# Kernel tuning notes

Measured on AMD Instinct MI355X. Metric: run time of the kernel, lower is better.

The kernel has to match this reference:

```python
import jax, jax.numpy as jnp
import numpy as np
from jax import lax

A = -0.75  # torch bicubic cubic-kernel coefficient

def _cubic(t):
    t = jnp.abs(t)
    return jnp.where(t <= 1.0, ((A + 2.0) * t - (A + 3.0)) * t * t + 1.0,
                     jnp.where(t < 2.0, A * (((t - 5.0) * t + 8.0) * t - 4.0), 0.0))

def _up2_1d(x, axis):
    # torch F.interpolate(scale_factor=2, mode='bicubic', align_corners=False) along one axis
    n = x.shape[axis]
    src = (jnp.arange(2 * n, dtype=jnp.float32) + 0.5) / 2.0 - 0.5
    i0 = jnp.floor(src).astype(jnp.int32)
    taps = i0[:, None] + jnp.arange(-1, 3)          # [2n,4]
    w = _cubic(src[:, None] - taps.astype(jnp.float32))
    g = jnp.take(x, jnp.clip(taps, 0, n - 1), axis=axis)  # clamp = border replicate
    wshape = [1] * g.ndim
    wshape[axis] = 2 * n
    wshape[axis + 1] = 4
    return jnp.sum(g * w.reshape(wshape), axis=axis + 1)

def bicubic_x2(x):
    return _up2_1d(_up2_1d(x, 2), 3)

def conv2d(x, w, b, stride=1, pad=0):
    y = lax.conv_general_dilated(x, w, (stride, stride), [(pad, pad), (pad, pad)],
                                 dimension_numbers=('NCHW', 'OIHW', 'NCHW'))
    return y + b[None, :, None, None]

def lrelu(x):
    return jax.nn.leaky_relu(x, 0.2)

def resblock(x, w1, b1, w2, b2):
    return x + conv2d(jax.nn.relu(conv2d(x, w1, b1, pad=1)), w2, b2, pad=1)

def feat_head(x, cw, cb, rw1, rb1, rw2, rb2):
    # Conv2d(3,32,5,p=2) -> LReLU -> ResBlock(32) -> LReLU
    return lrelu(resblock(lrelu(conv2d(x, cw, cb, pad=2)), rw1, rb1, rw2, rb2))

def setup_inputs() -> dict:
    key = jax.random.key(0)
    ks = jax.random.split(key, 16)
    def w(k, shape):
        fan = shape[1] * shape[2] * shape[3]
        return jax.random.normal(k, shape, jnp.float32) / np.sqrt(fan)
    def bvec(k, n):
        return jax.random.normal(k, (n,), jnp.float32) * 0.01
    return {
        'x':     jax.random.normal(ks[0], (1, 64, 320, 320), jnp.float32),
        'query': jax.random.normal(ks[1], (1, 3, 160, 160), jnp.float32),
        'ref':   jax.random.normal(ks[2], (1, 3, 320, 320), jnp.float32),
        'conv1_w': w(ks[3], (32, 3, 5, 5)),   'conv1_b': bvec(ks[4], 32),
        'r1_w1':   w(ks[5], (32, 32, 3, 3)),  'r1_b1':   bvec(ks[6], 32),
        'r1_w2':   w(ks[7], (32, 32, 3, 3)),  'r1_b2':   bvec(ks[8], 32),
        'p1_w':    w(ks[9], (32, 64, 5, 5)),  'p1_b':    bvec(ks[10], 32),
        'pr_w1':   w(ks[11], (32, 32, 3, 3)), 'pr_b1':   bvec(ks[12], 32),
        'pr_w2':   w(ks[13], (32, 32, 3, 3)), 'pr_b2':   bvec(ks[14], 32),
        'p2_w':    w(ks[15], (3, 32, 1, 1)),  'p2_b':    jnp.zeros((3,), jnp.float32),
    }

def reference(x, query, ref, conv1_w, conv1_b, r1_w1, r1_b1, r1_w2, r1_b2,
              p1_w, p1_b, pr_w1, pr_b1, pr_w2, pr_b2, p2_w, p2_b):
    ks = 2
    qf = feat_head(bicubic_x2(query), conv1_w, conv1_b, r1_w1, r1_b1, r1_w2, r1_b2)
    rf = feat_head(ref, conv1_w, conv1_b, r1_w1, r1_b1, r1_w2, r1_b2)
    feat = jnp.concatenate([rf, qf], axis=1)  # [b,64,h,w]
    hid = lrelu(resblock(lrelu(conv2d(feat, p1_w, p1_b, pad=2)), pr_w1, pr_b1, pr_w2, pr_b2))
    affine = conv2d(hid, p2_w, p2_b, pad=0) + 1.0   # [b,3,h,w]
    affine = jnp.clip(affine, -3.0, 3.0)
    xp = jnp.pad(x, ((0, 0), (0, 0), (1, 1), (1, 1)), mode='reflect')
    b, c, hp, wp = xp.shape
    h, w = affine.shape[2], affine.shape[3]
    aff = jnp.transpose(affine, (0, 2, 3, 1))       # [b,h,w,3]
    s_x, s_y = aff[..., 0:1], aff[..., 1:2]
    theta = (aff[..., 2:3] - 1.0) * 1.0472          # +/- 60 degrees
    # kernel grid (ks=2): meshgrid('ij') of [-0.5, 0.5], flattened
    pn_x = jnp.array([-0.5, -0.5, 0.5, 0.5], dtype=xp.dtype)
    pn_y = jnp.array([-0.5, 0.5, -0.5, 0.5], dtype=xp.dtype)
    px = pn_x * s_x                                  # [b,h,w,4]
    py = pn_y * s_y
    ct, st = jnp.cos(theta), jnp.sin(theta)
    # [px,py] @ [[c, s],[-s, c]]
    rx = px * ct - py * st
    ry = px * st + py * ct
    off = (ks - 1) // 2 + 0.5                        # 0.5
    p0x = jnp.arange(1, h + 1, dtype=xp.dtype)[None, :, None, None]
    p0y = jnp.arange(1, w + 1, dtype=xp.dtype)[None, None, :, None]
    p_x = rx + off + p0x
    p_y = ry + off + p0y
    lt_x = jnp.floor(lax.stop_gradient(p_x))
    lt_y = jnp.floor(lax.stop_gradient(p_y))
    rb_x, rb_y = lt_x + 1.0, lt_y + 1.0
    lt_xc = jnp.clip(lt_x, 0, hp - 1); lt_yc = jnp.clip(lt_y, 0, wp - 1)
    rb_xc = jnp.clip(rb_x, 0, hp - 1); rb_yc = jnp.clip(rb_y, 0, wp - 1)
    p_x = jnp.clip(p_x, 0, hp - 1); p_y = jnp.clip(p_y, 0, wp - 1)
    g_lt = (1.0 + lt_xc - p_x) * (1.0 + lt_yc - p_y)
    g_rb = (1.0 - (rb_xc - p_x)) * (1.0 - (rb_yc - p_y))
    g_lb = (1.0 + lt_xc - p_x) * (1.0 - (rb_yc - p_y))
    g_rt = (1.0 - (rb_xc - p_x)) * (1.0 + lt_yc - p_y)
    x_flat = xp.reshape(b, c, hp * wp)
    def gather(qx, qy):
        idx = qx.astype(jnp.int32) * wp + qy.astype(jnp.int32)  # [b,h,w,4]
        return jax.vmap(lambda xf, ix: xf[:, ix])(x_flat, idx)   # [b,c,h,w,4]
    align = (g_lt[:, None] * gather(lt_xc, lt_yc)
             + g_rb[:, None] * gather(rb_xc, rb_yc)
             + g_lb[:, None] * gather(lt_xc, rb_yc)
             + g_rt[:, None] * gather(rb_xc, lt_yc))
    # pixel-shuffle style reshape: N index = ix*ks + iy (from 'ij' meshgrid)
    out = align.reshape(b, c, h, w, ks, ks).transpose(0, 1, 2, 4, 3, 5).reshape(b, c, h * ks, w * ks)
    return out
```

## Files before the change

### kernel.cpp

```cpp
#include <hip/hip_runtime.h>

#define H 320
#define W 320
#define HW (H * W)
#define CH 64

typedef _Float16 f16;
typedef _Float16 f16x8 __attribute__((ext_vector_type(8)));
typedef float f32x16 __attribute__((ext_vector_type(16)));

__device__ __forceinline__ float cubw(float t) {
    t = fabsf(t);
    if (t <= 1.f) return (1.25f * t - 2.25f) * t * t + 1.f;
    if (t < 2.f)  return -0.75f * (((t - 5.f) * t + 8.f) * t - 4.f);
    return 0.f;
}

__global__ __launch_bounds__(256) void bicubic_k(const float* __restrict__ q,
                                                 float* __restrict__ outp) {
    int idx = blockIdx.x * 256 + threadIdx.x;
    if (idx >= 3 * HW) return;
    int c = idx / HW;
    int r = idx - c * HW;
    int oy = r / W, ox = r - (r / W) * W;
    float sy = oy * 0.5f - 0.25f;
    float sx = ox * 0.5f - 0.25f;
    int iy0 = (int)floorf(sy);
    int ix0 = (int)floorf(sx);
    float wy[4], wx[4];
    int tyi[4], txi[4];
#pragma unroll
    for (int a = 0; a < 4; a++) {
        int ty = iy0 - 1 + a;
        wy[a] = cubw(sy - (float)ty);
        tyi[a] = min(max(ty, 0), 159);
        int tx = ix0 - 1 + a;
        wx[a] = cubw(sx - (float)tx);
        txi[a] = min(max(tx, 0), 159);
    }
    const float* ip = q + c * (160 * 160);
    float o = 0.f;
#pragma unroll
    for (int b = 0; b < 4; b++) {
        float s = 0.f;
#pragma unroll
        for (int a = 0; a < 4; a++) s += wy[a] * ip[tyi[a] * 160 + txi[b]];
        o += wx[b] * s;
    }
    outp[idx] = o;
}

__global__ __launch_bounds__(256, 3) void hconv_k(const float* __restrict__ in0,
                                                  const float* __restrict__ in1,
                                                  const float* __restrict__ wgt,
                                                  const float* __restrict__ bias,
                                                  f16* __restrict__ out) {
    constexpr int KS = 5, PAD = 2;
    constexpr int TWX = 36, TWY = 36, TSTR = 37;
    constexpr int KS2 = 25, WSTR = 28;
    constexpr int ICB = 3, OCB = 4;

    __shared__ float tile[ICB][TWY][TSTR];
    __shared__ float wl[ICB][OCB][WSTR];

    const int bb = blockIdx.x >= 800 ? 1 : 0;
    const int bid = blockIdx.x - bb * 800;
    const float* in = bb ? in1 : in0;
    f16* o = out + (size_t)bb * (32 * HW);

    const int tid = threadIdx.x;
    const int tx = tid & 15, ty = tid >> 4;
    const int tileId = bid >> 3;
    const int oc0 = (bid & 7) * OCB;
    const int x0 = (tileId % 10) * 32;
    const int y0 = (tileId / 10) * 32;

    float acc[OCB][4];
#pragma unroll
    for (int i = 0; i < OCB; i++)
#pragma unroll
        for (int j = 0; j < 4; j++) acc[i][j] = 0.f;

    for (int idx = tid; idx < ICB * TWY * TWX; idx += 256) {
        int icc = idx / (TWY * TWX);
        int rem = idx - icc * (TWY * TWX);
        int r = rem / TWX, c = rem - r * TWX;
        int iy = y0 - PAD + r;
        int ix = x0 - PAD + c;
        float v = 0.f;
        if (iy >= 0 && iy < H && ix >= 0 && ix < W)
            v = in[icc * HW + iy * W + ix];
        tile[icc][r][c] = v;
    }
    for (int idx = tid; idx < ICB * OCB * KS2; idx += 256) {
        int icc = idx / (OCB * KS2);
        int rem = idx - icc * (OCB * KS2);
        int oc = rem / KS2, t = rem - oc * KS2;
        wl[icc][oc][t] = wgt[((oc0 + oc) * ICB + icc) * KS2 + t];
    }
    __syncthreads();

#pragma unroll
    for (int icc = 0; icc < ICB; ++icc) {
        float win[2][KS][KS + 1];
#pragma unroll
        for (int h = 0; h < 2; h++)
#pragma unroll
            for (int r = 0; r < KS; r++)
#pragma unroll
                for (int c = 0; c < KS + 1; c++)
                    win[h][r][c] = tile[icc][ty + 16 * h + r][2 * tx + c];
#pragma unroll
        for (int oc = 0; oc < OCB; ++oc) {
            float wv[KS2];
#pragma unroll
            for (int t = 0; t < KS2; t++) wv[t] = wl[icc][oc][t];
#pragma unroll
            for (int h = 0; h < 2; h++)
#pragma unroll
                for (int r = 0; r < KS; r++)
#pragma unroll
                    for (int c = 0; c < KS; c++) {
                        acc[oc][2 * h]     += win[h][r][c]     * wv[r * KS + c];
                        acc[oc][2 * h + 1] += win[h][r][c + 1] * wv[r * KS + c];
                    }
        }
    }

    const int col = x0 + 2 * tx;
#pragma unroll
    for (int oc = 0; oc < OCB; ++oc) {
        float bv = bias[oc0 + oc];
#pragma unroll
        for (int h = 0; h < 2; h++) {
            int row = y0 + ty + 16 * h;
            int pix = row * W + col;
#pragma unroll
            for (int c2 = 0; c2 < 2; c2++) {
                float v = acc[oc][2 * h + c2] + bv;
                v = (v > 0.f) ? v : 0.2f * v;
                o[(pix + c2) * 32 + oc0 + oc] = (f16)v;
            }
        }
    }
}

__global__ __launch_bounds__(256) void repack_k(const float* __restrict__ w0,
                                                const float* __restrict__ w1,
                                                const float* __restrict__ w2,
                                                const float* __restrict__ w3,
                                                const float* __restrict__ w4,
                                                f16* __restrict__ dst) {
    int li = blockIdx.x * 256 + threadIdx.x;
    const float* src;
    int CIN, KS2, base, rel;
    if (li < 1152)       { src = w0; CIN = 32; KS2 = 9;  base = 0;     rel = li; }
    else if (li < 2304)  { src = w1; CIN = 32; KS2 = 9;  base = 9216;  rel = li - 1152; }
    else if (li < 3456)  { src = w2; CIN = 32; KS2 = 9;  base = 18432; rel = li - 2304; }
    else if (li < 4608)  { src = w3; CIN = 32; KS2 = 9;  base = 27648; rel = li - 3456; }
    else if (li < 11008) { src = w4; CIN = 64; KS2 = 25; base = 36864; rel = li - 4608; }
    else return;
    int fi = rel >> 6, l = rel & 63;
    int kc = fi / KS2, t = fi - kc * KS2;
    int oc = l & 31, kh = l >> 5;
#pragma unroll
    for (int i = 0; i < 8; ++i) {
        int ic = kc * 16 + kh * 8 + i;
        dst[base + rel * 8 + i] = (f16)src[(oc * CIN + ic) * KS2 + t];
    }
}

template <int KS, int CIN, int ACT, bool RES>
__global__ __launch_bounds__(256) void mconv_k(const f16* __restrict__ in,
                                               const f16* __restrict__ wrep,
                                               const float* __restrict__ bias,
                                               const f16* __restrict__ res,
                                               f16* __restrict__ out,
                                               int OUTC, int inStr, int resStr,
                                               int outStr, int oc0Base, int oc0Step) {
    constexpr int PAD = KS / 2;
    constexpr int TY = 8 + 2 * PAD;
    constexpr int TX = 32 + 2 * PAD;
    constexpr int NPX = TY * TX;
    constexpr int NU = CIN / 4;
    constexpr int UM = NU - 1;
    constexpr int KC = CIN / 16;
    constexpr int KS2 = KS * KS;

    __shared__ uint2 lds2[NPX * NU];

    const int b = blockIdx.x >= 400 ? 1 : 0;
    const int tb = blockIdx.x - b * 400;
    in  += (size_t)b * inStr;
    res += (size_t)b * resStr;
    out += (size_t)b * outStr;
    const int oc0 = oc0Base + b * oc0Step;

    const int tid = threadIdx.x;
    const int bx = tb % 10;
    const int by = tb / 10;
    const int x0 = bx * 32, y0 = by * 8;

    {
        const int cu = tid & UM;
        constexpr int STEP = 256 / NU;
        for (int p = tid / NU; p < NPX; p += STEP) {
            int ly = p / TX, lx = p - ly * TX;
            int gy = y0 - PAD + ly, gx = x0 - PAD + lx;
            uint2 v; v.x = 0u; v.y = 0u;
            if (gy >= 0 && gy < H && gx >= 0 && gx < W)
                v = *reinterpret_cast<const uint2*>(in + (gy * W + gx) * CIN + cu * 4);
            lds2[p * NU + (cu ^ (p & UM))] = v;
        }
    }
    __syncthreads();

    const int lane = tid & 63;
    const int wv = tid >> 6;
    const int R = lane & 31;
    const int hh = lane >> 5;

    f32x16 acc0, acc1;
#pragma unroll
    for (int j = 0; j < 16; ++j) { acc0[j] = 0.f; acc1[j] = 0.f; }

#pragma unroll
    for (int kc = 0; kc < KC; ++kc) {
#pragma unroll
        for (int t = 0; t < KS2; ++t) {
            const int dy = t / KS, dx = t - dy * KS;
            f16x8 B = *reinterpret_cast<const f16x8*>(
                wrep + ((kc * KS2 + t) * 64 + lane) * 8);
            const int u0 = (kc * 2 + hh) * 2;
            {
                int p = (2 * wv + 0 + dy) * TX + R + dx;
                union { uint2 u[2]; f16x8 v; } A;
                A.u[0] = lds2[p * NU + ((u0)     ^ (p & UM))];
                A.u[1] = lds2[p * NU + ((u0 + 1) ^ (p & UM))];
                acc0 = __builtin_amdgcn_mfma_f32_32x32x16_f16(A.v, B, acc0, 0, 0, 0);
            }
            {
                int p = (2 * wv + 1 + dy) * TX + R + dx;
                union { uint2 u[2]; f16x8 v; } A;
                A.u[0] = lds2[p * NU + ((u0)     ^ (p & UM))];
                A.u[1] = lds2[p * NU + ((u0 + 1) ^ (p & UM))];
                acc1 = __builtin_amdgcn_mfma_f32_32x32x16_f16(A.v, B, acc1, 0, 0, 0);
            }
        }
    }

    const float bv = bias[R];
#pragma unroll
    for (int m = 0; m < 2; ++m) {
        const int gy = y0 + 2 * wv + m;
        f32x16 a = m ? acc1 : acc0;
#pragma unroll
        for (int r = 0; r < 16; ++r) {
            int X = x0 + (r & 3) + 8 * (r >> 2) + 4 * hh;
            int pix = gy * W + X;
            float v = a[r] + bv;
            if constexpr (RES) v += (float)res[pix * 32 + R];
            if constexpr (ACT == 0) v = fmaxf(v, 0.f);
            else                    v = (v > 0.f) ? v : 0.2f * v;
            out[pix * OUTC + oc0 + R] = (f16)v;
        }
    }
}

__global__ __launch_bounds__(256) void affine_k(const f16* __restrict__ hid,
                                                const float* __restrict__ w,
                                                const float* __restrict__ b,
                                                float* __restrict__ outp) {
    int p = blockIdx.x * 256 + threadIdx.x;
    if (p >= HW) return;
    const f16x8* hv = reinterpret_cast<const f16x8*>(hid + p * 32);
    float a0 = 0.f, a1 = 0.f, a2 = 0.f;
#pragma unroll
    for (int cc = 0; cc < 4; ++cc) {
        f16x8 hb = hv[cc];
#pragma unroll
        for (int j = 0; j < 8; ++j) {
            float hval = (float)hb[j];
            int c = cc * 8 + j;
            a0 += hval * w[c];
            a1 += hval * w[32 + c];
            a2 += hval * w[64 + c];
        }
    }
    a0 = fminf(fmaxf(a0 + b[0] + 1.f, -3.f), 3.f);
    a1 = fminf(fmaxf(a1 + b[1] + 1.f, -3.f), 3.f);
    a2 = fminf(fmaxf(a2 + b[2] + 1.f, -3.f), 3.f);
    outp[p] = a0;
    outp[HW + p] = a1;
    outp[2 * HW + p] = a2;
}

__device__ __forceinline__ int reflmap(int q) {
    int s = q - 1;
    if (s < 0) s = -s;
    else if (s > 319) s = 638 - s;
    return s;
}

__global__ __launch_bounds__(256) void sample_k(const float* __restrict__ x,
                                                const float* __restrict__ aff,
                                                float* __restrict__ outp) {
    __shared__ float tile[16 * 6 * 96];
    int bid = blockIdx.x;
    bid = (bid & 7) * 800 + (bid >> 3);
    const int cg = bid / 1600;
    const int tb = bid - cg * 1600;
    const int h = tb / 5;
    const int q = tb - 5 * h;
    const int tid = threadIdx.x;
    const int ow = q * 128 + (tid & 127);
    const int oh = 2 * h + (tid >> 7);

    const int w = ow >> 1;
    const int ky = ow & 1, kx = oh & 1;
    const int p = h * W + w;
    float s_x = aff[p];
    float s_y = aff[HW + p];
    float th = (aff[2 * HW + p] - 1.f) * 1.0472f;
    float pnx = kx ? 0.5f : -0.5f;
    float pny = ky ? 0.5f : -0.5f;
    float px = pnx * s_x, py = pny * s_y;
    float st, ct;
    __sincosf(th, &st, &ct);
    float rx = px * ct - py * st;
    float ry = px * st + py * ct;
    float p_x = rx + 0.5f + (float)(h + 1);
    float p_y = ry + 0.5f + (float)(w + 1);
    float ltx = floorf(p_x), lty = floorf(p_y);
    float rbx = ltx + 1.f, rby = lty + 1.f;
    float ltxc = fminf(fmaxf(ltx, 0.f), 321.f);
    float ltyc = fminf(fmaxf(lty, 0.f), 321.f);
    float rbxc = fminf(fmaxf(rbx, 0.f), 321.f);
    float rbyc = fminf(fmaxf(rby, 0.f), 321.f);
    p_x = fminf(fmaxf(p_x, 0.f), 321.f);
    p_y = fminf(fmaxf(p_y, 0.f), 321.f);
    float gx0 = 1.f + ltxc - p_x;
    float gx1 = 1.f - (rbxc - p_x);
    float gy0 = 1.f + ltyc - p_y;
    float gy1 = 1.f - (rbyc - p_y);
    float g_lt = gx0 * gy0, g_rb = gx1 * gy1, g_lb = gx0 * gy1, g_rt = gx1 * gy0;
    int ix0 = reflmap((int)ltxc), ix1 = reflmap((int)rbxc);
    int iy0 = reflmap((int)ltyc), iy1 = reflmap((int)rbyc);

    const int rowbase = h - 2;
    const int colbase = q * 64 - 4;
    const int o00 = (ix0 - rowbase) * 96 + (iy0 - colbase);
    const int o01 = (ix0 - rowbase) * 96 + (iy1 - colbase);
    const int o10 = (ix1 - rowbase) * 96 + (iy0 - colbase);
    const int o11 = (ix1 - rowbase) * 96 + (iy1 - colbase);
    const int obase = oh * 640 + ow;
    const int ch0 = cg * 16;

    for (int idx = tid; idx < 1728; idx += 256) {
        int ch = idx / 108;
        int rem = idx - ch * 108;
        int row = rem / 18;
        int g = rem - row * 18;
        int rv = rowbase + row;
        int cv = colbase + 4 * g;
        float4 v = make_float4(0.f, 0.f, 0.f, 0.f);
        if (rv >= 0 && rv < H && cv >= 0 && cv < W)
            v = *reinterpret_cast<const float4*>(x + (size_t)(ch0 + ch) * HW + rv * W + cv);
        *reinterpret_cast<float4*>(&tile[ch * 576 + row * 96 + 4 * g]) = v;
    }
    __syncthreads();

#pragma unroll
    for (int c = 0; c < 16; ++c) {
        const float* t = tile + c * 576;
        float v = g_lt * t[o00] + g_rb * t[o11] + g_lb * t[o01] + g_rt * t[o10];
        __builtin_nontemporal_store(v, outp + (size_t)(ch0 + c) * (640 * 640) + obase);
    }
}

extern "C" void kernel_launch(void* const* d_in, const int* in_sizes, int n_in,
                              void* d_out, int out_size, void* d_ws, size_t ws_size,
                              hipStream_t stream) {
    const float* x       = (const float*)d_in[0];
    const float* query   = (const float*)d_in[1];
    const float* ref     = (const float*)d_in[2];
    const float* conv1_w = (const float*)d_in[3];
    const float* conv1_b = (const float*)d_in[4];
    const float* r1_w1   = (const float*)d_in[5];
    const float* r1_b1   = (const float*)d_in[6];
    const float* r1_w2   = (const float*)d_in[7];
    const float* r1_b2   = (const float*)d_in[8];
    const float* p1_w    = (const float*)d_in[9];
    const float* p1_b    = (const float*)d_in[10];
    const float* pr_w1   = (const float*)d_in[11];
    const float* pr_b1   = (const float*)d_in[12];
    const float* pr_w2   = (const float*)d_in[13];
    const float* pr_b2   = (const float*)d_in[14];
    const float* p2_w    = (const float*)d_in[15];
    const float* p2_b    = (const float*)d_in[16];

    float* outp = (float*)d_out;
    float* ws = (float*)d_ws;

    float* qup    = ws;
    float* affine = ws + 3 * HW;
    f16* feat = (f16*)outp;
    f16* Bt   = (f16*)(outp + 32 * HW);
    f16* Ct   = (f16*)(outp + 64 * HW);
    f16* Dt   = (f16*)(outp + 96 * HW);
    f16* wrep = (f16*)(outp + 112 * HW);

    repack_k<<<43, 256, 0, stream>>>(r1_w1, r1_w2, pr_w1, pr_w2, p1_w, wrep);
    bicubic_k<<<1200, 256, 0, stream>>>(query, qup);

    hconv_k<<<1600, 256, 0, stream>>>(qup, ref, conv1_w, conv1_b, Bt);
    mconv_k<3, 32, 0, false><<<800, 256, 0, stream>>>(Bt, wrep,        r1_b1, nullptr, Ct,
                                                      32, 32 * HW, 0, 32 * HW, 0, 0);
    mconv_k<3, 32, 1, true ><<<800, 256, 0, stream>>>(Ct, wrep + 9216, r1_b2, Bt, feat,
                                                      64, 32 * HW, 32 * HW, 0, 32, -32);

    mconv_k<5, 64, 1, false><<<400, 256, 0, stream>>>(feat, wrep + 36864, p1_b, nullptr, Bt,
                                                      32, 0, 0, 0, 0, 0);
    mconv_k<3, 32, 0, false><<<400, 256, 0, stream>>>(Bt, wrep + 18432, pr_b1, nullptr, Ct,
                                                      32, 0, 0, 0, 0, 0);
    mconv_k<3, 32, 1, true ><<<400, 256, 0, stream>>>(Ct, wrep + 27648, pr_b2, Bt, Dt,
                                                      32, 0, 0, 0, 0, 0);

    affine_k<<<400, 256, 0, stream>>>(Dt, p2_w, p2_b, affine);

    sample_k<<<6400, 256, 0, stream>>>(x, affine, outp);
}
```

Measured before the change: 308.4 us.

## Rewrite 5x5 head conv as MFMA im2col matmul and shrink sampler tile

The first 3-to-32 channel 5x5 convolution moves from scalar FP32 FMAs to MFMA 32x32x16 f16 instructions. It uses an im2col-style A operand built from an LDS input tile, and the weights are repacked into a padded K=80 f16 layout inside the existing repack kernel. The per-block tile becomes 8 rows by 32 columns covering all 32 output channels, which halves the grid. Separately, the sampler's shared-memory tile row stride drops from 96 to 80 floats, reducing LDS footprint to allow more resident blocks. The trade-off is f16 rounding of inputs and weights for the head conv, plus scattered LDS reads when building A fragments.

```diff
diff --git a/kernel.cpp b/kernel.cpp
--- a/kernel.cpp
+++ b/kernel.cpp
@@ -50,116 +50,38 @@
     outp[idx] = o;
 }
 
-__global__ __launch_bounds__(256, 3) void hconv_k(const float* __restrict__ in0,
-                                                  const float* __restrict__ in1,
-                                                  const float* __restrict__ wgt,
-                                                  const float* __restrict__ bias,
-                                                  f16* __restrict__ out) {
-    constexpr int KS = 5, PAD = 2;
-    constexpr int TWX = 36, TWY = 36, TSTR = 37;
-    constexpr int KS2 = 25, WSTR = 28;
-    constexpr int ICB = 3, OCB = 4;
-
-    __shared__ float tile[ICB][TWY][TSTR];
-    __shared__ float wl[ICB][OCB][WSTR];
-
-    const int bb = blockIdx.x >= 800 ? 1 : 0;
-    const int bid = blockIdx.x - bb * 800;
-    const float* in = bb ? in1 : in0;
-    f16* o = out + (size_t)bb * (32 * HW);
-
-    const int tid = threadIdx.x;
-    const int tx = tid & 15, ty = tid >> 4;
-    const int tileId = bid >> 3;
-    const int oc0 = (bid & 7) * OCB;
-    const int x0 = (tileId % 10) * 32;
-    const int y0 = (tileId / 10) * 32;
-
-    float acc[OCB][4];
-#pragma unroll
-    for (int i = 0; i < OCB; i++)
-#pragma unroll
-        for (int j = 0; j < 4; j++) acc[i][j] = 0.f;
-
-    for (int idx = tid; idx < ICB * TWY * TWX; idx += 256) {
-        int icc = idx / (TWY * TWX);
-        int rem = idx - icc * (TWY * TWX);
-        int r = rem / TWX, c = rem - r * TWX;
-        int iy = y0 - PAD + r;
-        int ix = x0 - PAD + c;
-        float v = 0.f;
-        if (iy >= 0 && iy < H && ix >= 0 && ix < W)
-            v = in[icc * HW + iy * W + ix];
-        tile[icc][r][c] = v;
-    }
-    for (int idx = tid; idx < ICB * OCB * KS2; idx += 256) {
-        int icc = idx / (OCB * KS2);
-        int rem = idx - icc * (OCB * KS2);
-        int oc = rem / KS2, t = rem - oc * KS2;
-        wl[icc][oc][t] = wgt[((oc0 + oc) * ICB + icc) * KS2 + t];
-    }
-    __syncthreads();
-
-#pragma unroll
-    for (int icc = 0; icc < ICB; ++icc) {
-        float win[2][KS][KS + 1];
-#pragma unroll
-        for (int h = 0; h < 2; h++)
-#pragma unroll
-            for (int r = 0; r < KS; r++)
-#pragma unroll
-                for (int c = 0; c < KS + 1; c++)
-                    win[h][r][c] = tile[icc][ty + 16 * h + r][2 * tx + c];
-#pragma unroll
-        for (int oc = 0; oc < OCB; ++oc) {
-            float wv[KS2];
-#pragma unroll
-            for (int t = 0; t < KS2; t++) wv[t] = wl[icc][oc][t];
-#pragma unroll
-            for (int h = 0; h < 2; h++)
-#pragma unroll
-                for (int r = 0; r < KS; r++)
-#pragma unroll
-                    for (int c = 0; c < KS; c++) {
-                        acc[oc][2 * h]     += win[h][r][c]     * wv[r * KS + c];
-                        acc[oc][2 * h + 1] += win[h][r][c + 1] * wv[r * KS + c];
-                    }
-        }
-    }
-
-    const int col = x0 + 2 * tx;
-#pragma unroll
-    for (int oc = 0; oc < OCB; ++oc) {
-        float bv = bias[oc0 + oc];
-#pragma unroll
-        for (int h = 0; h < 2; h++) {
-            int row = y0 + ty + 16 * h;
-            int pix = row * W + col;
-#pragma unroll
-            for (int c2 = 0; c2 < 2; c2++) {
-                float v = acc[oc][2 * h + c2] + bv;
-                v = (v > 0.f) ? v : 0.2f * v;
-                o[(pix + c2) * 32 + oc0 + oc] = (f16)v;
-            }
-        }
-    }
-}
-
 __global__ __launch_bounds__(256) void repack_k(const float* __restrict__ w0,
                                                 const float* __restrict__ w1,
                                                 const float* __restrict__ w2,
                                                 const float* __restrict__ w3,
                                                 const float* __restrict__ w4,
+                                                const float* __restrict__ w5,
                                                 f16* __restrict__ dst) {
     int li = blockIdx.x * 256 + threadIdx.x;
+    if (li >= 11328) return;
+    if (li >= 11008) {
+        int rel = li - 11008;
+        int kc = rel >> 6, l = rel & 63;
+        int oc = l & 31, kh = l >> 5;
+#pragma unroll
+        for (int i = 0; i < 8; ++i) {
+            int k = kc * 16 + kh * 8 + i;
+            f16 v = (f16)0.f;
+            if (k < 75) {
+                int tap = k / 3, ic = k - 3 * tap;
+                v = (f16)w5[(oc * 3 + ic) * 25 + tap];
+            }
+            dst[88064 + rel * 8 + i] = v;
+        }
+        return;
+    }
     const float* src;
     int CIN, KS2, base, rel;
     if (li < 1152)       { src = w0; CIN = 32; KS2 = 9;  base = 0;     rel = li; }
     else if (li < 2304)  { src = w1; CIN = 32; KS2 = 9;  base = 9216;  rel = li - 1152; }
     else if (li < 3456)  { src = w2; CIN = 32; KS2 = 9;  base = 18432; rel = li - 2304; }
     else if (li < 4608)  { src = w3; CIN = 32; KS2 = 9;  base = 27648; rel = li - 3456; }
-    else if (li < 11008) { src = w4; CIN = 64; KS2 = 25; base = 36864; rel = li - 4608; }
-    else return;
+    else                 { src = w4; CIN = 64; KS2 = 25; base = 36864; rel = li - 4608; }
     int fi = rel >> 6, l = rel & 63;
     int kc = fi / KS2, t = fi - kc * KS2;
     int oc = l & 31, kh = l >> 5;
@@ -167,6 +89,75 @@
     for (int i = 0; i < 8; ++i) {
         int ic = kc * 16 + kh * 8 + i;
         dst[base + rel * 8 + i] = (f16)src[(oc * CIN + ic) * KS2 + t];
+    }
+}
+
+__global__ __launch_bounds__(256) void hconv_m(const float* __restrict__ in0,
+                                               const float* __restrict__ in1,
+                                               const f16* __restrict__ wr5,
+                                               const float* __restrict__ bias,
+                                               f16* __restrict__ out) {
+    __shared__ float tile[3][12][40];
+    const int b = blockIdx.x >= 400 ? 1 : 0;
+    const int tb = blockIdx.x - b * 400;
+    const float* in = b ? in1 : in0;
+    f16* o = out + (size_t)b * (32 * HW);
+    const int x0 = (tb % 10) * 32, y0 = (tb / 10) * 8;
+    const int tid = threadIdx.x;
+
+    for (int idx = tid; idx < 1440; idx += 256) {
+        int ic = idx / 480;
+        int rem = idx - ic * 480;
+        int r = rem / 40, c = rem - r * 40;
+        int gy = y0 - 2 + r, gx = x0 - 2 + c;
+        float v = 0.f;
+        if (gy >= 0 && gy < H && gx >= 0 && gx < W)
+            v = in[ic * HW + gy * W + gx];
+        tile[ic][r][c] = v;
+    }
+    __syncthreads();
+
+    const int lane = tid & 63, wv = tid >> 6;
+    const int R = lane & 31, hh = lane >> 5;
+
+    f32x16 acc0, acc1;
+#pragma unroll
+    for (int j = 0; j < 16; ++j) { acc0[j] = 0.f; acc1[j] = 0.f; }
+
+#pragma unroll
+    for (int kc = 0; kc < 5; ++kc) {
+        f16x8 B = *reinterpret_cast<const f16x8*>(wr5 + (kc * 64 + lane) * 8);
+#pragma unroll
+        for (int m = 0; m < 2; ++m) {
+            f16x8 A;
+#pragma unroll
+            for (int i = 0; i < 8; ++i) {
+                int k = kc * 16 + hh * 8 + i;
+                float v = 0.f;
+                if (k < 75) {
+                    int tap = k / 3, ic = k - 3 * tap;
+                    int dy = tap / 5, dx = tap - 5 * dy;
+                    v = tile[ic][2 * wv + m + dy][R + dx];
+                }
+                A[i] = (f16)v;
+            }
+            if (m == 0) acc0 = __builtin_amdgcn_mfma_f32_32x32x16_f16(A, B, acc0, 0, 0, 0);
+            else        acc1 = __builtin_amdgcn_mfma_f32_32x32x16_f16(A, B, acc1, 0, 0, 0);
+        }
+    }
+
+    const float bv = bias[R];
+#pragma unroll
+    for (int m = 0; m < 2; ++m) {
+        const int gy = y0 + 2 * wv + m;
+        f32x16 a = m ? acc1 : acc0;
+#pragma unroll
+        for (int r = 0; r < 16; ++r) {
+            int X = x0 + (r & 3) + 8 * (r >> 2) + 4 * hh;
+            float v = a[r] + bv;
+            v = (v > 0.f) ? v : 0.2f * v;
+            o[(gy * W + X) * 32 + R] = (f16)v;
+        }
     }
 }
 
@@ -305,7 +296,7 @@
 __global__ __launch_bounds__(256) void sample_k(const float* __restrict__ x,
                                                 const float* __restrict__ aff,
                                                 float* __restrict__ outp) {
-    __shared__ float tile[16 * 6 * 96];
+    __shared__ float tile[16 * 6 * 80];
     int bid = blockIdx.x;
     bid = (bid & 7) * 800 + (bid >> 3);
     const int cg = bid / 1600;
@@ -349,10 +340,10 @@
 
     const int rowbase = h - 2;
     const int colbase = q * 64 - 4;
-    const int o00 = (ix0 - rowbase) * 96 + (iy0 - colbase);
-    const int o01 = (ix0 - rowbase) * 96 + (iy1 - colbase);
-    const int o10 = (ix1 - rowbase) * 96 + (iy0 - colbase);
-    const int o11 = (ix1 - rowbase) * 96 + (iy1 - colbase);
+    const int o00 = (ix0 - rowbase) * 80 + (iy0 - colbase);
+    const int o01 = (ix0 - rowbase) * 80 + (iy1 - colbase);
+    const int o10 = (ix1 - rowbase) * 80 + (iy0 - colbase);
+    const int o11 = (ix1 - rowbase) * 80 + (iy1 - colbase);
     const int obase = oh * 640 + ow;
     const int ch0 = cg * 16;
 
@@ -366,13 +357,13 @@
         float4 v = make_float4(0.f, 0.f, 0.f, 0.f);
         if (rv >= 0 && rv < H && cv >= 0 && cv < W)
             v = *reinterpret_cast<const float4*>(x + (size_t)(ch0 + ch) * HW + rv * W + cv);
-        *reinterpret_cast<float4*>(&tile[ch * 576 + row * 96 + 4 * g]) = v;
+        *reinterpret_cast<float4*>(&tile[ch * 480 + row * 80 + 4 * g]) = v;
     }
     __syncthreads();
 
 #pragma unroll
     for (int c = 0; c < 16; ++c) {
-        const float* t = tile + c * 576;
+        const float* t = tile + c * 480;
         float v = g_lt * t[o00] + g_rb * t[o11] + g_lb * t[o01] + g_rt * t[o10];
         __builtin_nontemporal_store(v, outp + (size_t)(ch0 + c) * (640 * 640) + obase);
     }
@@ -410,10 +401,10 @@
     f16* Dt   = (f16*)(outp + 96 * HW);
     f16* wrep = (f16*)(outp + 112 * HW);
 
-    repack_k<<<43, 256, 0, stream>>>(r1_w1, r1_w2, pr_w1, pr_w2, p1_w, wrep);
+    repack_k<<<45, 256, 0, stream>>>(r1_w1, r1_w2, pr_w1, pr_w2, p1_w, conv1_w, wrep);
     bicubic_k<<<1200, 256, 0, stream>>>(query, qup);
 
-    hconv_k<<<1600, 256, 0, stream>>>(qup, ref, conv1_w, conv1_b, Bt);
+    hconv_m<<<800, 256, 0, stream>>>(qup, ref, wrep + 88064, conv1_b, Bt);
     mconv_k<3, 32, 0, false><<<800, 256, 0, stream>>>(Bt, wrep,        r1_b1, nullptr, Ct,
                                                       32, 32 * HW, 0, 32 * HW, 0, 0);
     mconv_k<3, 32, 1, true ><<<800, 256, 0, stream>>>(Ct, wrep + 9216, r1_b2, Bt, feat,
```

Result: faster. 273.4 us (-11.3%).
